# Kernel optimization log

Hardware: AMD Instinct MI355X
Metric: run time of the kernel (lower is better)

## Reference

```python
import jax, jax.numpy as jnp
import numpy as np

M = 2048
K = 512


def setup_inputs() -> dict:
    key = jax.random.key(0)
    k1, k2, k3, k4, k5 = jax.random.split(key, 5)
    inputs = jax.random.normal(k1, (16384, M), dtype=jnp.float32)
    # MyLinear(m, k): weight [k, m], bias [k] (torch Linear convention)
    s1 = 1.0 / np.sqrt(M)
    s2 = 1.0 / np.sqrt(K)
    W1 = jax.random.uniform(k2, (K, M), jnp.float32, -s1, s1)
    b1 = jax.random.uniform(k3, (K,), jnp.float32, -s1, s1)
    W2 = jax.random.uniform(k4, (M, K), jnp.float32, -s2, s2)
    b2 = jax.random.uniform(k5, (M,), jnp.float32, -s2, s2)
    return {"inputs": inputs, "W1": W1, "b1": b1, "W2": W2, "b2": b2}


def reference(inputs, W1, b1, W2, b2):
    # Original loops per sample; math is identical to one batched chain:
    # hidden = x @ W1^T + b1 ; out = hidden @ W2^T + b2 (no nonlinearity)
    hidden = jnp.einsum("bm,km->bk", inputs, W1) + b1  # [B, K]
    out = jnp.einsum("bk,mk->bm", hidden, W2) + b2     # [B, M]
    return out
```

## Files before the change

### kernel.cpp

```cpp
#include <hip/hip_runtime.h>
#include <hip/hip_bf16.h>
#include <stdint.h>


typedef short bf16x8 __attribute__((ext_vector_type(8)));
typedef float f32x4 __attribute__((ext_vector_type(4)));

static __device__ __forceinline__ unsigned short f32_to_bf16_rne(float f) {
    unsigned int u = __float_as_uint(f);
    u += 0x7fffu + ((u >> 16) & 1u);
    return (unsigned short)(u >> 16);
}

static __device__ __forceinline__ unsigned int cvt_pk_bf16(float lo, float hi) {
    unsigned int r;
    asm("v_cvt_pk_bf16_f32 %0, %1, %2" : "=v"(r) : "v"(lo), "v"(hi));
    return r;
}

__global__ void cast_f32_to_bf16(const float* __restrict__ in,
                                 unsigned short* __restrict__ out, int n4) {
    int stride = gridDim.x * blockDim.x;
    for (int i = blockIdx.x * blockDim.x + threadIdx.x; i < n4; i += stride) {
        float4 v = ((const float4*)in)[i];
        ushort4 o;
        o.x = f32_to_bf16_rne(v.x);
        o.y = f32_to_bf16_rne(v.y);
        o.z = f32_to_bf16_rne(v.z);
        o.w = f32_to_bf16_rne(v.w);
        ((ushort4*)out)[i] = o;
    }
}

#define GLOAD_LDS16(gsrc, ldst)                                              \
    __builtin_amdgcn_global_load_lds(                                        \
        (const __attribute__((address_space(1))) void*)(gsrc),               \
        (__attribute__((address_space(3))) void*)(ldst), 16, 0, 0)

__global__ __launch_bounds__(256)
void gemm1_xcast(const float* __restrict__ X,
                 const unsigned short* __restrict__ W1,
                 const float* __restrict__ b1,
                 unsigned short* __restrict__ H) {
    constexpr int K = 2048, N = 512, BK = 64, NSTEP = K / BK;

    __shared__ __align__(16) unsigned short ldsX[128 * BK];
    __shared__ __align__(16) unsigned short ldsW[128 * BK];

    const int tid  = threadIdx.x;
    const int lane = tid & 63;
    const int wid  = tid >> 6;
    const int wr   = wid >> 1;
    const int wc   = wid & 1;

    const int bid = blockIdx.x;
    const int swz = ((bid & 7) << 6) + (bid >> 3);
    const int bm  = swz >> 2;
    const int bn  = swz & 3;
    const int brow = bm << 7;
    const int bcol = bn << 7;

    const int lrow = lane & 15;
    const int ku   = lane >> 4;
    const int rx   = lrow & 7;

    const int srow = tid >> 3;
    const int sgu  = (tid & 7) ^ (srow & 7);
    const float* xptr = X + (size_t)(brow + srow) * K + ((tid & 7) << 3);
    const int xlds = srow * 128 + (((tid & 7) ^ (srow & 7)) << 4);

    f32x4 acc[4][4] = {};
    f32x4 xv[4][2];

    auto loadX = [&](int k0) {
#pragma unroll
        for (int j = 0; j < 4; ++j) {
            const float* p = xptr + (size_t)j * 32 * K + k0;
            xv[j][0] = *(const f32x4*)p;
            xv[j][1] = *(const f32x4*)(p + 4);
        }
    };
    auto writeX = [&]() {
#pragma unroll
        for (int j = 0; j < 4; ++j) {
            uint4 u;
            u.x = cvt_pk_bf16(xv[j][0][0], xv[j][0][1]);
            u.y = cvt_pk_bf16(xv[j][0][2], xv[j][0][3]);
            u.z = cvt_pk_bf16(xv[j][1][0], xv[j][1][1]);
            u.w = cvt_pk_bf16(xv[j][1][2], xv[j][1][3]);
            *(uint4*)((char*)ldsX + j * 4096 + xlds) = u;
        }
    };
    auto stageW = [&](int k0) {
#pragma unroll
        for (int i = 0; i < 4; ++i) {
            const char* src =
                (const char*)(W1 + (size_t)(bcol + i * 32 + srow) * K + k0) + (sgu << 4);
            GLOAD_LDS16(src, (char*)ldsW + i * 4096 + tid * 16);
        }
    };
    auto compute = [&]() {
#pragma unroll
        for (int kk = 0; kk < 2; ++kk) {
            const int un = ((ku + (kk << 2)) ^ rx) << 4;
            bf16x8 a[4], b[4];
#pragma unroll
            for (int m = 0; m < 4; ++m)
                a[m] = *(const bf16x8*)((const char*)ldsX +
                       ((wr << 6) + (m << 4) + lrow) * 128 + un);
#pragma unroll
            for (int n = 0; n < 4; ++n)
                b[n] = *(const bf16x8*)((const char*)ldsW +
                       ((wc << 6) + (n << 4) + lrow) * 128 + un);
#pragma unroll
            for (int m = 0; m < 4; ++m)
#pragma unroll
                for (int n = 0; n < 4; ++n)
                    acc[m][n] = __builtin_amdgcn_mfma_f32_16x16x32_bf16(
                        a[m], b[n], acc[m][n], 0, 0, 0);
        }
    };

    loadX(0);
    stageW(0);
    writeX();
    __syncthreads();

    for (int t = 0; t < NSTEP; ++t) {
        const bool more = (t + 1 < NSTEP);
        if (more) loadX((t + 1) * BK);
        compute();
        if (more) {
            __syncthreads();
            stageW((t + 1) * BK);
            writeX();
            __syncthreads();
        }
    }

    const int r0 = (lane >> 4) << 2;
#pragma unroll
    for (int n = 0; n < 4; ++n) {
        const int col = bcol + (wc << 6) + (n << 4) + lrow;
        const float bb = b1[col];
#pragma unroll
        for (int m = 0; m < 4; ++m)
#pragma unroll
            for (int j = 0; j < 4; ++j) {
                const int row = brow + (wr << 6) + (m << 4) + r0 + j;
                H[(size_t)row * N + col] = f32_to_bf16_rne(acc[m][n][j] + bb);
            }
    }
}

__global__ __launch_bounds__(256)
void gemm2(const unsigned short* __restrict__ A,
           const unsigned short* __restrict__ Bt,
           const float* __restrict__ bias,
           float* __restrict__ C) {
    constexpr int N = 2048, Kd = 512, BK = 64, NSTEP = Kd / BK;

    __shared__ __align__(16) unsigned short ldsA[128 * BK];
    __shared__ __align__(16) unsigned short ldsB[128 * BK];

    const int tid  = threadIdx.x;
    const int lane = tid & 63;
    const int wid  = tid >> 6;
    const int wr   = wid >> 1;
    const int wc   = wid & 1;

    const int bid = blockIdx.x;
    const int swz = ((bid & 7) << 8) + (bid >> 3);
    const int bn  = swz & 15;
    const int bm  = swz >> 4;
    const int brow = bm << 7;
    const int bcol = bn << 7;

    const int lrow = lane & 15;
    const int ku   = lane >> 4;
    const int rx   = lrow & 7;

    const int srow = tid >> 3;
    const int sgu  = (tid & 7) ^ (srow & 7);

    f32x4 acc[4][4] = {};

    auto stage = [&](int k0) {
#pragma unroll
        for (int i = 0; i < 4; ++i) {
            const int row = i * 32 + srow;
            const char* sa =
                (const char*)(A + (size_t)(brow + row) * Kd + k0) + (sgu << 4);
            const char* sb =
                (const char*)(Bt + (size_t)(bcol + row) * Kd + k0) + (sgu << 4);
            GLOAD_LDS16(sa, (char*)ldsA + i * 4096 + tid * 16);
            GLOAD_LDS16(sb, (char*)ldsB + i * 4096 + tid * 16);
        }
    };
    auto compute = [&]() {
#pragma unroll
        for (int kk = 0; kk < 2; ++kk) {
            const int un = ((ku + (kk << 2)) ^ rx) << 4;
            bf16x8 a[4], b[4];
#pragma unroll
            for (int m = 0; m < 4; ++m)
                a[m] = *(const bf16x8*)((const char*)ldsA +
                       ((wr << 6) + (m << 4) + lrow) * 128 + un);
#pragma unroll
            for (int n = 0; n < 4; ++n)
                b[n] = *(const bf16x8*)((const char*)ldsB +
                       ((wc << 6) + (n << 4) + lrow) * 128 + un);
#pragma unroll
            for (int m = 0; m < 4; ++m)
#pragma unroll
                for (int n = 0; n < 4; ++n)
                    acc[m][n] = __builtin_amdgcn_mfma_f32_16x16x32_bf16(
                        a[m], b[n], acc[m][n], 0, 0, 0);
        }
    };

    stage(0);
    __syncthreads();

    for (int t = 0; t < NSTEP; ++t) {
        compute();
        if (t + 1 < NSTEP) {
            __syncthreads();
            stage((t + 1) * BK);
            __syncthreads();
        }
    }

    const int r0 = (lane >> 4) << 2;
#pragma unroll
    for (int n = 0; n < 4; ++n) {
        const int col = bcol + (wc << 6) + (n << 4) + lrow;
        const float bb = bias[col];
#pragma unroll
        for (int m = 0; m < 4; ++m)
#pragma unroll
            for (int j = 0; j < 4; ++j) {
                const int row = brow + (wr << 6) + (m << 4) + r0 + j;
                C[(size_t)row * N + col] = acc[m][n][j] + bb;
            }
    }
}

extern "C" void kernel_launch(void* const* d_in, const int* in_sizes, int n_in,
                              void* d_out, int out_size, void* d_ws, size_t ws_size,
                              hipStream_t stream) {
    const float* X  = (const float*)d_in[0];
    const float* W1 = (const float*)d_in[1];
    const float* b1 = (const float*)d_in[2];
    const float* W2 = (const float*)d_in[3];
    const float* b2 = (const float*)d_in[4];

    const int B = 16384, M = 2048, Kd = 512;

    char* ws = (char*)d_ws;
    unsigned short* W1bf = (unsigned short*)ws;
    unsigned short* W2bf = W1bf + (size_t)Kd * M;
    unsigned short* Hbf  = W2bf + (size_t)M * Kd;

    cast_f32_to_bf16<<<1024, 256, 0, stream>>>(W1, W1bf, Kd * M / 4);
    cast_f32_to_bf16<<<1024, 256, 0, stream>>>(W2, W2bf, M * Kd / 4);

    gemm1_xcast<<<(B / 128) * (Kd / 128), 256, 0, stream>>>(X, W1bf, b1, Hbf);
    gemm2<<<(B / 128) * (M / 128), 256, 0, stream>>>(Hbf, W2bf, b2, (float*)d_out);
}
```

Baseline: 140.0 us.

## Double-buffer gemm1 LDS with 512-thread blocks and merge weight cast kernels

gemm1 now runs 8 waves per block, each computing a 64x32 sub-tile, and uses double-buffered LDS for X and W1. The next tile's global loads and bf16 conversion overlap compute on the current buffer, which cuts the barriers per K-step from two to one. The two weight-cast launches are merged into one kernel to save a launch. The price is double the LDS per block and a smaller per-wave tile, so each wave does less MFMA work per LDS read.

```diff
diff --git a/kernel.cpp b/kernel.cpp
--- a/kernel.cpp
+++ b/kernel.cpp
@@ -18,17 +18,23 @@
     return r;
 }
 
-__global__ void cast_f32_to_bf16(const float* __restrict__ in,
-                                 unsigned short* __restrict__ out, int n4) {
+__global__ void cast_weights_bf16(const float* __restrict__ w1,
+                                  unsigned short* __restrict__ o1,
+                                  const float* __restrict__ w2,
+                                  unsigned short* __restrict__ o2, int n4each) {
     int stride = gridDim.x * blockDim.x;
-    for (int i = blockIdx.x * blockDim.x + threadIdx.x; i < n4; i += stride) {
-        float4 v = ((const float4*)in)[i];
+    for (int i = blockIdx.x * blockDim.x + threadIdx.x; i < 2 * n4each;
+         i += stride) {
+        const float* in = (i < n4each) ? w1 : w2;
+        unsigned short* out = (i < n4each) ? o1 : o2;
+        int j = (i < n4each) ? i : i - n4each;
+        float4 v = ((const float4*)in)[j];
         ushort4 o;
         o.x = f32_to_bf16_rne(v.x);
         o.y = f32_to_bf16_rne(v.y);
         o.z = f32_to_bf16_rne(v.z);
         o.w = f32_to_bf16_rne(v.w);
-        ((ushort4*)out)[i] = o;
+        ((ushort4*)out)[j] = o;
     }
 }
 
@@ -37,21 +43,21 @@
         (const __attribute__((address_space(1))) void*)(gsrc),               \
         (__attribute__((address_space(3))) void*)(ldst), 16, 0, 0)
 
-__global__ __launch_bounds__(256)
+__global__ __launch_bounds__(512, 4)
 void gemm1_xcast(const float* __restrict__ X,
                  const unsigned short* __restrict__ W1,
                  const float* __restrict__ b1,
                  unsigned short* __restrict__ H) {
     constexpr int K = 2048, N = 512, BK = 64, NSTEP = K / BK;
 
-    __shared__ __align__(16) unsigned short ldsX[128 * BK];
-    __shared__ __align__(16) unsigned short ldsW[128 * BK];
+    __shared__ __align__(16) unsigned short ldsX[2][128 * BK];
+    __shared__ __align__(16) unsigned short ldsW[2][128 * BK];
 
     const int tid  = threadIdx.x;
     const int lane = tid & 63;
     const int wid  = tid >> 6;
-    const int wr   = wid >> 1;
-    const int wc   = wid & 1;
+    const int wr   = wid >> 2;
+    const int wc   = wid & 3;
 
     const int bid = blockIdx.x;
     const int swz = ((bid & 7) << 6) + (bid >> 3);
@@ -64,84 +70,96 @@
     const int ku   = lane >> 4;
     const int rx   = lrow & 7;
 
-    const int srow = tid >> 3;
-    const int sgu  = (tid & 7) ^ (srow & 7);
-    const float* xptr = X + (size_t)(brow + srow) * K + ((tid & 7) << 3);
-    const int xlds = srow * 128 + (((tid & 7) ^ (srow & 7)) << 4);
-
-    f32x4 acc[4][4] = {};
-    f32x4 xv[4][2];
+    const int xrow = tid >> 2;
+    const int xu0  = (tid & 3) << 1;
+    const float* xptr = X + (size_t)(brow + xrow) * K + (xu0 << 3);
+    const int xb0 = xrow * 128 + ((xu0 ^ (xrow & 7)) << 4);
+    const int xb1 = xrow * 128 + (((xu0 | 1) ^ (xrow & 7)) << 4);
+
+    const int wrow0 = tid >> 3;
+    const int wu    = tid & 7;
+
+    f32x4 acc[4][2] = {};
+    f32x4 xv[4];
 
     auto loadX = [&](int k0) {
-#pragma unroll
-        for (int j = 0; j < 4; ++j) {
-            const float* p = xptr + (size_t)j * 32 * K + k0;
-            xv[j][0] = *(const f32x4*)p;
-            xv[j][1] = *(const f32x4*)(p + 4);
-        }
-    };
-    auto writeX = [&]() {
-#pragma unroll
-        for (int j = 0; j < 4; ++j) {
-            uint4 u;
-            u.x = cvt_pk_bf16(xv[j][0][0], xv[j][0][1]);
-            u.y = cvt_pk_bf16(xv[j][0][2], xv[j][0][3]);
-            u.z = cvt_pk_bf16(xv[j][1][0], xv[j][1][1]);
-            u.w = cvt_pk_bf16(xv[j][1][2], xv[j][1][3]);
-            *(uint4*)((char*)ldsX + j * 4096 + xlds) = u;
-        }
-    };
-    auto stageW = [&](int k0) {
-#pragma unroll
-        for (int i = 0; i < 4; ++i) {
-            const char* src =
-                (const char*)(W1 + (size_t)(bcol + i * 32 + srow) * K + k0) + (sgu << 4);
-            GLOAD_LDS16(src, (char*)ldsW + i * 4096 + tid * 16);
-        }
-    };
-    auto compute = [&]() {
+        const float* p = xptr + k0;
+        xv[0] = *(const f32x4*)p;
+        xv[1] = *(const f32x4*)(p + 4);
+        xv[2] = *(const f32x4*)(p + 8);
+        xv[3] = *(const f32x4*)(p + 12);
+    };
+    auto writeX = [&](unsigned short* bufX) {
+        uint4 a, b;
+        a.x = cvt_pk_bf16(xv[0][0], xv[0][1]);
+        a.y = cvt_pk_bf16(xv[0][2], xv[0][3]);
+        a.z = cvt_pk_bf16(xv[1][0], xv[1][1]);
+        a.w = cvt_pk_bf16(xv[1][2], xv[1][3]);
+        b.x = cvt_pk_bf16(xv[2][0], xv[2][1]);
+        b.y = cvt_pk_bf16(xv[2][2], xv[2][3]);
+        b.z = cvt_pk_bf16(xv[3][0], xv[3][1]);
+        b.w = cvt_pk_bf16(xv[3][2], xv[3][3]);
+        *(uint4*)((char*)bufX + xb0) = a;
+        *(uint4*)((char*)bufX + xb1) = b;
+    };
+    auto stageW = [&](int k0, unsigned short* bufW) {
+#pragma unroll
+        for (int i = 0; i < 2; ++i) {
+            const int row = i * 64 + wrow0;
+            const char* src = (const char*)(W1 + (size_t)(bcol + row) * K + k0)
+                              + ((wu ^ (row & 7)) << 4);
+            GLOAD_LDS16(src, (char*)bufW + i * 8192 + tid * 16);
+        }
+    };
+    auto compute = [&](const unsigned short* bufX, const unsigned short* bufW) {
 #pragma unroll
         for (int kk = 0; kk < 2; ++kk) {
             const int un = ((ku + (kk << 2)) ^ rx) << 4;
-            bf16x8 a[4], b[4];
-#pragma unroll
-            for (int m = 0; m < 4; ++m)
-                a[m] = *(const bf16x8*)((const char*)ldsX +
+            bf16x8 a[4], b[2];
+#pragma unroll
+            for (int m = 0; m < 4; ++m)
+                a[m] = *(const bf16x8*)((const char*)bufX +
                        ((wr << 6) + (m << 4) + lrow) * 128 + un);
 #pragma unroll
-            for (int n = 0; n < 4; ++n)
-                b[n] = *(const bf16x8*)((const char*)ldsW +
-                       ((wc << 6) + (n << 4) + lrow) * 128 + un);
-#pragma unroll
-            for (int m = 0; m < 4; ++m)
-#pragma unroll
-                for (int n = 0; n < 4; ++n)
+            for (int n = 0; n < 2; ++n)
+                b[n] = *(const bf16x8*)((const char*)bufW +
+                       ((wc << 5) + (n << 4) + lrow) * 128 + un);
+#pragma unroll
+            for (int m = 0; m < 4; ++m)
+#pragma unroll
+                for (int n = 0; n < 2; ++n)
                     acc[m][n] = __builtin_amdgcn_mfma_f32_16x16x32_bf16(
                         a[m], b[n], acc[m][n], 0, 0, 0);
         }
     };
 
     loadX(0);
-    stageW(0);
-    writeX();
+    stageW(0, ldsW[0]);
+    writeX(ldsX[0]);
     __syncthreads();
 
-    for (int t = 0; t < NSTEP; ++t) {
-        const bool more = (t + 1 < NSTEP);
-        if (more) loadX((t + 1) * BK);
-        compute();
+#pragma unroll 1
+    for (int t = 0; t < NSTEP; t += 2) {
+        loadX((t + 1) * BK);
+        stageW((t + 1) * BK, ldsW[1]);
+        compute(ldsX[0], ldsW[0]);
+        writeX(ldsX[1]);
+        __syncthreads();
+
+        const bool more = (t + 2 < NSTEP);
         if (more) {
-            __syncthreads();
-            stageW((t + 1) * BK);
-            writeX();
-            __syncthreads();
-        }
+            loadX((t + 2) * BK);
+            stageW((t + 2) * BK, ldsW[0]);
+        }
+        compute(ldsX[1], ldsW[1]);
+        if (more) writeX(ldsX[0]);
+        __syncthreads();
     }
 
     const int r0 = (lane >> 4) << 2;
 #pragma unroll
-    for (int n = 0; n < 4; ++n) {
-        const int col = bcol + (wc << 6) + (n << 4) + lrow;
+    for (int n = 0; n < 2; ++n) {
+        const int col = bcol + (wc << 5) + (n << 4) + lrow;
         const float bb = b1[col];
 #pragma unroll
         for (int m = 0; m < 4; ++m)
@@ -262,9 +280,10 @@
     unsigned short* W2bf = W1bf + (size_t)Kd * M;
     unsigned short* Hbf  = W2bf + (size_t)M * Kd;
 
-    cast_f32_to_bf16<<<1024, 256, 0, stream>>>(W1, W1bf, Kd * M / 4);
-    cast_f32_to_bf16<<<1024, 256, 0, stream>>>(W2, W2bf, M * Kd / 4);
-
-    gemm1_xcast<<<(B / 128) * (Kd / 128), 256, 0, stream>>>(X, W1bf, b1, Hbf);
-    gemm2<<<(B / 128) * (M / 128), 256, 0, stream>>>(Hbf, W2bf, b2, (float*)d_out);
-}
+    cast_weights_bf16<<<2048, 256, 0, stream>>>(W1, W1bf, W2, W2bf,
+                                                Kd * M / 4);
+
+    gemm1_xcast<<<(B / 128) * (Kd / 128), 512, 0, stream>>>(X, W1bf, b1, Hbf);
+    gemm2<<<(B / 128) * (M / 128), 256, 0, stream>>>(Hbf, W2bf, b2,
+                                                     (float*)d_out);
+}
```

Result: faster. 133.2 us (-4.8%).

## Stage fp32 X directly to LDS via async loads and convert at fragment read

Applied to the files above, without the earlier changes.

In gemm1, the X tile is no longer loaded into registers, converted to bf16 and written to LDS. It is now copied as fp32 straight into LDS with global_load_lds, using a swizzled layout, and converted to bf16 when the MFMA fragments are read. This removes the register round-trip and the VGPR pressure from holding the prefetched X, and it adds a launch bound of 2 blocks per CU. The cost is that the X LDS tile doubles to 32KB, the conversion is repeated for each wave's reads, and the prefetch overlap the old register staging gave is lost. The two weight cast kernels are also merged into one launch.

```diff
diff --git a/kernel.cpp b/kernel.cpp
--- a/kernel.cpp
+++ b/kernel.cpp
@@ -18,17 +18,23 @@
     return r;
 }
 
-__global__ void cast_f32_to_bf16(const float* __restrict__ in,
-                                 unsigned short* __restrict__ out, int n4) {
+__global__ void cast_weights_bf16(const float* __restrict__ w1,
+                                  unsigned short* __restrict__ o1,
+                                  const float* __restrict__ w2,
+                                  unsigned short* __restrict__ o2, int n4each) {
     int stride = gridDim.x * blockDim.x;
-    for (int i = blockIdx.x * blockDim.x + threadIdx.x; i < n4; i += stride) {
-        float4 v = ((const float4*)in)[i];
+    for (int i = blockIdx.x * blockDim.x + threadIdx.x; i < 2 * n4each;
+         i += stride) {
+        const float* in = (i < n4each) ? w1 : w2;
+        unsigned short* out = (i < n4each) ? o1 : o2;
+        int j = (i < n4each) ? i : i - n4each;
+        float4 v = ((const float4*)in)[j];
         ushort4 o;
         o.x = f32_to_bf16_rne(v.x);
         o.y = f32_to_bf16_rne(v.y);
         o.z = f32_to_bf16_rne(v.z);
         o.w = f32_to_bf16_rne(v.w);
-        ((ushort4*)out)[i] = o;
+        ((ushort4*)out)[j] = o;
     }
 }
 
@@ -37,14 +43,14 @@
         (const __attribute__((address_space(1))) void*)(gsrc),               \
         (__attribute__((address_space(3))) void*)(ldst), 16, 0, 0)
 
-__global__ __launch_bounds__(256)
+__global__ __launch_bounds__(256, 2)
 void gemm1_xcast(const float* __restrict__ X,
                  const unsigned short* __restrict__ W1,
                  const float* __restrict__ b1,
                  unsigned short* __restrict__ H) {
     constexpr int K = 2048, N = 512, BK = 64, NSTEP = K / BK;
 
-    __shared__ __align__(16) unsigned short ldsX[128 * BK];
+    __shared__ __align__(16) float ldsX[128 * BK];
     __shared__ __align__(16) unsigned short ldsW[128 * BK];
 
     const int tid  = threadIdx.x;
@@ -62,56 +68,51 @@
 
     const int lrow = lane & 15;
     const int ku   = lane >> 4;
-    const int rx   = lrow & 7;
-
-    const int srow = tid >> 3;
-    const int sgu  = (tid & 7) ^ (srow & 7);
-    const float* xptr = X + (size_t)(brow + srow) * K + ((tid & 7) << 3);
-    const int xlds = srow * 128 + (((tid & 7) ^ (srow & 7)) << 4);
+
+    const int xr  = tid >> 4;
+    const int xsw = ((tid & 15) ^ xr) << 4;
+    const char* xsrc0 = (const char*)(X + (size_t)(brow + xr) * K) + xsw;
+
+    const int wrr = tid >> 3;
+    const int wsw = ((tid & 7) ^ (wrr & 7)) << 4;
+    const char* wsrc0 = (const char*)(W1 + (size_t)(bcol + wrr) * K) + wsw;
 
     f32x4 acc[4][4] = {};
-    f32x4 xv[4][2];
-
-    auto loadX = [&](int k0) {
-#pragma unroll
-        for (int j = 0; j < 4; ++j) {
-            const float* p = xptr + (size_t)j * 32 * K + k0;
-            xv[j][0] = *(const f32x4*)p;
-            xv[j][1] = *(const f32x4*)(p + 4);
-        }
-    };
-    auto writeX = [&]() {
-#pragma unroll
-        for (int j = 0; j < 4; ++j) {
-            uint4 u;
-            u.x = cvt_pk_bf16(xv[j][0][0], xv[j][0][1]);
-            u.y = cvt_pk_bf16(xv[j][0][2], xv[j][0][3]);
-            u.z = cvt_pk_bf16(xv[j][1][0], xv[j][1][1]);
-            u.w = cvt_pk_bf16(xv[j][1][2], xv[j][1][3]);
-            *(uint4*)((char*)ldsX + j * 4096 + xlds) = u;
-        }
-    };
-    auto stageW = [&](int k0) {
-#pragma unroll
-        for (int i = 0; i < 4; ++i) {
-            const char* src =
-                (const char*)(W1 + (size_t)(bcol + i * 32 + srow) * K + k0) + (sgu << 4);
-            GLOAD_LDS16(src, (char*)ldsW + i * 4096 + tid * 16);
-        }
-    };
+
+    auto stage = [&](int k0) {
+#pragma unroll
+        for (int i = 0; i < 8; ++i)
+            GLOAD_LDS16(xsrc0 + ((size_t)i * 16 * K + k0) * 4,
+                        (char*)ldsX + i * 4096 + tid * 16);
+#pragma unroll
+        for (int i = 0; i < 4; ++i)
+            GLOAD_LDS16(wsrc0 + ((size_t)i * 32 * K + k0) * 2,
+                        (char*)ldsW + i * 4096 + tid * 16);
+    };
+
     auto compute = [&]() {
 #pragma unroll
         for (int kk = 0; kk < 2; ++kk) {
-            const int un = ((ku + (kk << 2)) ^ rx) << 4;
+            const int luA = (ku + (kk << 2)) << 1;
+            const int unW = ((ku + (kk << 2)) ^ (lrow & 7)) << 4;
             bf16x8 a[4], b[4];
 #pragma unroll
-            for (int m = 0; m < 4; ++m)
-                a[m] = *(const bf16x8*)((const char*)ldsX +
-                       ((wr << 6) + (m << 4) + lrow) * 128 + un);
+            for (int m = 0; m < 4; ++m) {
+                const int ra = (wr << 6) + (m << 4) + lrow;
+                const char* base = (const char*)ldsX + ra * 256;
+                f32x4 lo = *(const f32x4*)(base + ((luA ^ lrow) << 4));
+                f32x4 hi = *(const f32x4*)(base + (((luA + 1) ^ lrow) << 4));
+                uint4 u;
+                u.x = cvt_pk_bf16(lo[0], lo[1]);
+                u.y = cvt_pk_bf16(lo[2], lo[3]);
+                u.z = cvt_pk_bf16(hi[0], hi[1]);
+                u.w = cvt_pk_bf16(hi[2], hi[3]);
+                a[m] = *(const bf16x8*)&u;
+            }
 #pragma unroll
             for (int n = 0; n < 4; ++n)
                 b[n] = *(const bf16x8*)((const char*)ldsW +
-                       ((wc << 6) + (n << 4) + lrow) * 128 + un);
+                       ((wc << 6) + (n << 4) + lrow) * 128 + unW);
 #pragma unroll
             for (int m = 0; m < 4; ++m)
 #pragma unroll
@@ -121,19 +122,14 @@
         }
     };
 
-    loadX(0);
-    stageW(0);
-    writeX();
+    stage(0);
     __syncthreads();
 
     for (int t = 0; t < NSTEP; ++t) {
-        const bool more = (t + 1 < NSTEP);
-        if (more) loadX((t + 1) * BK);
         compute();
-        if (more) {
-            __syncthreads();
-            stageW((t + 1) * BK);
-            writeX();
+        if (t + 1 < NSTEP) {
+            __syncthreads();
+            stage((t + 1) * BK);
             __syncthreads();
         }
     }
@@ -262,9 +258,10 @@
     unsigned short* W2bf = W1bf + (size_t)Kd * M;
     unsigned short* Hbf  = W2bf + (size_t)M * Kd;
 
-    cast_f32_to_bf16<<<1024, 256, 0, stream>>>(W1, W1bf, Kd * M / 4);
-    cast_f32_to_bf16<<<1024, 256, 0, stream>>>(W2, W2bf, M * Kd / 4);
+    cast_weights_bf16<<<2048, 256, 0, stream>>>(W1, W1bf, W2, W2bf,
+                                                Kd * M / 4);
 
     gemm1_xcast<<<(B / 128) * (Kd / 128), 256, 0, stream>>>(X, W1bf, b1, Hbf);
-    gemm2<<<(B / 128) * (M / 128), 256, 0, stream>>>(Hbf, W2bf, b2, (float*)d_out);
-}
+    gemm2<<<(B / 128) * (M / 128), 256, 0, stream>>>(Hbf, W2bf, b2,
+                                                     (float*)d_out);
+}
```

Result: faster. 126.6 us (-9.6%).
